# Performance work log

Hardware: AMD Instinct MI355X
Metric: run time of the kernel (lower is better)

Reference implementation:

```python
import jax, jax.numpy as jnp
import numpy as np

L, H, C = 2, 2, 128            # conv layers, heads, out_channels
N, E, B = 10000, 100000, 64    # nodes, edges, graphs
F_NODE, F_EDGE, FC = 92, 50, 512
HC, C3 = H * C, 3 * C


def _ln(x, g, b, eps=1e-5):
    m = x.mean(-1, keepdims=True)
    v = jnp.var(x, axis=-1, keepdims=True)
    return (x - m) * jax.lax.rsqrt(v + eps) * g + b


def setup_inputs() -> dict:
    key = jax.random.key(0)
    ks = jax.random.split(key, 20)
    r = lambda i, shape, s=0.05: jax.random.normal(ks[i], shape, jnp.float32) * s
    d = {}
    d["x"] = jax.random.normal(ks[0], (N, F_NODE), jnp.float32)
    d["edge_attr"] = jax.random.normal(ks[1], (E, F_EDGE), jnp.float32)
    d["pge"] = jax.random.normal(ks[2], (B, 32), jnp.float32)
    d["cse"] = jax.random.normal(ks[3], (B, 7), jnp.float32)
    d["edge_index"] = jax.random.randint(ks[4], (2, E), 0, N, jnp.int32)
    d["batch"] = jnp.sort(jax.random.randint(ks[5], (N,), 0, B, jnp.int32))
    d["atom_W"] = r(6, (F_NODE, C)); d["atom_b"] = jnp.zeros(C)
    d["edge_W"] = r(7, (F_EDGE, C)); d["edge_b"] = jnp.zeros(C)
    d["Wq"] = r(8, (L, C, HC)); d["bq"] = jnp.zeros((L, HC))
    d["Wk"] = r(9, (L, C, HC)); d["bk"] = jnp.zeros((L, HC))
    d["Wv"] = r(10, (L, C, HC)); d["bv"] = jnp.zeros((L, HC))
    d["We"] = r(11, (L, C, HC))
    d["Wmu"] = r(12, (L, C3, C3)); d["bmu"] = jnp.zeros((L, C3))
    d["Wm"] = r(13, (L, C3, C)); d["bm"] = jnp.zeros((L, C))
    d["ln_m_g"] = jnp.ones((L, C)); d["ln_m_b"] = jnp.zeros((L, C))
    d["ln_a_g"] = jnp.ones((L, C3)); d["ln_a_b"] = jnp.zeros((L, C3))
    d["Wc"] = r(14, (L, HC, C)); d["bc"] = jnp.zeros((L, C))
    d["bn_g"] = jnp.ones((L, C)); d["bn_b"] = jnp.zeros((L, C))
    d["Wskip"] = r(15, (L, C, C)); d["bskip"] = jnp.zeros((L, C))
    d["fc_W"] = r(16, (C + 32 + 7, FC)); d["fc_b"] = jnp.zeros(FC)
    d["out_W"] = r(17, (FC, 1)); d["out_b"] = jnp.zeros(1)
    return d


def reference(x, edge_attr, pge, cse, edge_index, batch, atom_W, atom_b,
              edge_W, edge_b, Wq, bq, Wk, bk, Wv, bv, We, Wmu, bmu, Wm, bm,
              ln_m_g, ln_m_b, ln_a_g, ln_a_b, Wc, bc, bn_g, bn_b, Wskip,
              bskip, fc_W, fc_b, out_W, out_b):
    src, dst = edge_index[0], edge_index[1]  # j = source, i = target
    nf = x @ atom_W + atom_b                 # [N, C]
    ef = edge_attr @ edge_W + edge_b         # [E, C]
    scale = 1.0 / np.sqrt(C3).astype(np.float32)
    for i in range(L):
        q = (nf @ Wq[i] + bq[i]).reshape(N, H, C)
        k = (nf @ Wk[i] + bk[i]).reshape(N, H, C)
        v = (nf @ Wv[i] + bv[i]).reshape(N, H, C)
        ea = (ef @ We[i]).reshape(E, H, C)
        qi = q[dst]
        qcat = jnp.concatenate([qi, qi, qi], -1)                 # [E,H,3C]
        kcat = jnp.concatenate([k[dst], k[src], ea], -1)         # [E,H,3C]
        alpha = qcat * kcat * scale
        gate = jax.nn.sigmoid(_ln(alpha, ln_a_g[i], ln_a_b[i]))
        m = jnp.concatenate([v[dst], v[src], ea], -1)            # [E,H,3C]
        m = (jnp.einsum('ehf,fg->ehg', m, Wmu[i]) + bmu[i]) * gate
        m = jnp.einsum('ehf,fc->ehc', m, Wm[i]) + bm[i]          # [E,H,C]
        m = _ln(m, ln_m_g[i], ln_m_b[i])
        agg = jax.ops.segment_sum(m, dst, num_segments=N)        # scatter-add
        o = agg.reshape(N, HC) @ Wc[i] + bc[i]                   # lin_concate
        mu = o.mean(0); var = jnp.var(o, axis=0)                 # BN (batch stats)
        o = (o - mu) * jax.lax.rsqrt(var + 1e-5) * bn_g[i] + bn_b[i]
        o = jax.nn.silu(o)
        nf = o + nf @ Wskip[i] + bskip[i]                        # root skip
    sums = jax.ops.segment_sum(nf, batch, num_segments=B)
    cnt = jax.ops.segment_sum(jnp.ones((N, 1), nf.dtype), batch, num_segments=B)
    pooled = sums / jnp.maximum(cnt, 1.0)                        # global_mean_pool
    feats = jnp.concatenate([pooled, pge, cse], 1)               # [B, C+39]
    h = jax.nn.silu(feats @ fc_W + fc_b)
    return h @ out_W + out_b                                     # [B, 1]
```

## Files before the change

kernel.cpp:

```cpp
#include <hip/hip_runtime.h>
#include <math.h>

#define N_NODES 10000
#define N_EDGES 100000
#define N_GRAPH 64
#define CDIM 128
#define HCDIM 256
#define C3DIM 384
#define QKPW 2176

typedef unsigned short u16;
typedef __attribute__((ext_vector_type(8))) short bf16x8;
typedef __attribute__((ext_vector_type(4))) float f32x4;

__device__ __forceinline__ u16 f2bf(float f) {
  union { float f; unsigned int u; } x; x.f = f;
  unsigned int u = x.u + 0x7fffu + ((x.u >> 16) & 1u);
  return (u16)(u >> 16);
}
__device__ __forceinline__ float bf2f(u16 h) {
  union { unsigned int u; float f; } x; x.u = ((unsigned int)h) << 16;
  return x.f;
}

template<int OUT_BF16, int DO_STATS, int A_F32>
__global__ __launch_bounds__(256) void mfma_gemm_kernel(
    const void* __restrict__ Ain, const u16* __restrict__ WT,
    const float* __restrict__ bias, void* __restrict__ Y,
    u16* __restrict__ Ymirror, float* __restrict__ cs, float* __restrict__ cs2,
    int M, int K, int N) {
  const int tid = threadIdx.x;
  const int w = tid >> 6, l = tid & 63;
  const int lq = l >> 4, ln = l & 15;
  const int bm = blockIdx.y * 128, bn = blockIdx.x * 64;
  int ra = bm + w * 32 + ln;      if (ra > M - 1) ra = M - 1;
  int rb = bm + w * 32 + 16 + ln; if (rb > M - 1) rb = M - 1;
  f32x4 acc[2][4];
#pragma unroll
  for (int g = 0; g < 2; ++g)
#pragma unroll
    for (int nt = 0; nt < 4; ++nt) acc[g][nt] = {0.f, 0.f, 0.f, 0.f};
  for (int k0 = 0; k0 < K; k0 += 32) {
    bf16x8 a0, a1;
    if (A_F32) {
      const float* Af = (const float*)Ain;
      f32x4 p0 = *(const f32x4*)&Af[(size_t)ra * K + k0 + lq * 8];
      f32x4 p1 = *(const f32x4*)&Af[(size_t)ra * K + k0 + lq * 8 + 4];
      f32x4 p2 = *(const f32x4*)&Af[(size_t)rb * K + k0 + lq * 8];
      f32x4 p3 = *(const f32x4*)&Af[(size_t)rb * K + k0 + lq * 8 + 4];
#pragma unroll
      for (int j = 0; j < 4; ++j) {
        a0[j] = (short)f2bf(p0[j]); a0[4 + j] = (short)f2bf(p1[j]);
        a1[j] = (short)f2bf(p2[j]); a1[4 + j] = (short)f2bf(p3[j]);
      }
    } else {
      const u16* Ab = (const u16*)Ain;
      a0 = *(const bf16x8*)&Ab[(size_t)ra * K + k0 + lq * 8];
      a1 = *(const bf16x8*)&Ab[(size_t)rb * K + k0 + lq * 8];
    }
#pragma unroll
    for (int nt = 0; nt < 4; ++nt) {
      bf16x8 b = *(const bf16x8*)&WT[(size_t)(bn + nt * 16 + ln) * K + k0 + lq * 8];
      acc[0][nt] = __builtin_amdgcn_mfma_f32_16x16x32_bf16(a0, b, acc[0][nt], 0, 0, 0);
      acc[1][nt] = __builtin_amdgcn_mfma_f32_16x16x32_bf16(a1, b, acc[1][nt], 0, 0, 0);
    }
  }
#pragma unroll
  for (int g = 0; g < 2; ++g) {
    int rowbase = bm + w * 32 + g * 16 + lq * 4;
#pragma unroll
    for (int nt = 0; nt < 4; ++nt) {
      int gn = bn + nt * 16 + ln;
      float bv = bias ? bias[gn] : 0.f;
#pragma unroll
      for (int r = 0; r < 4; ++r) {
        int gm = rowbase + r;
        if (gm < M) {
          float val = acc[g][nt][r] + bv;
          if (OUT_BF16) ((u16*)Y)[(size_t)gm * N + gn] = f2bf(val);
          else          ((float*)Y)[(size_t)gm * N + gn] = val;
          if (Ymirror)  Ymirror[(size_t)gm * N + gn] = f2bf(val);
        }
      }
    }
  }
  if (DO_STATS) {
#pragma unroll
    for (int nt = 0; nt < 4; ++nt) {
      int gn = bn + nt * 16 + ln;
      float bv = bias ? bias[gn] : 0.f;
      float s = 0.f, s2 = 0.f;
#pragma unroll
      for (int g = 0; g < 2; ++g) {
        int rowbase = bm + w * 32 + g * 16 + lq * 4;
#pragma unroll
        for (int r = 0; r < 4; ++r) {
          if (rowbase + r < M) {
            float v = acc[g][nt][r] + bv;
            s += v; s2 += v * v;
          }
        }
      }
      s += __shfl_xor(s, 16); s2 += __shfl_xor(s2, 16);
      s += __shfl_xor(s, 32); s2 += __shfl_xor(s2, 32);
      if (lq == 0) { atomicAdd(&cs[gn], s); atomicAdd(&cs2[gn], s2); }
    }
  }
}

__global__ void pack_init_kernel(
    const float* __restrict__ x, const float* __restrict__ ea,
    const float* __restrict__ atom_W, const float* __restrict__ edge_W,
    u16* __restrict__ xpad, u16* __restrict__ epad,
    u16* __restrict__ atomWT, u16* __restrict__ WeT2) {
  int z = blockIdx.y;
  int idx0 = blockIdx.x * 256 + threadIdx.x;
  const int stride = 256 * 256;
  if (z == 0) {
    for (int idx = idx0; idx < N_NODES * 96; idx += stride) {
      int n = idx / 96, k = idx - n * 96;
      xpad[idx] = (k < 92) ? f2bf(x[(size_t)n * 92 + k]) : (u16)0;
    }
  } else if (z == 1) {
    for (int idx = idx0; idx < N_EDGES * 64; idx += stride) {
      int e = idx >> 6, k = idx & 63;
      epad[idx] = (k < 50) ? f2bf(ea[(size_t)e * 50 + k]) : (u16)0;
    }
  } else if (z == 2) {
    if (idx0 < 128 * 96) { int n = idx0 / 96, k = idx0 - n * 96;
      atomWT[idx0] = (k < 92) ? f2bf(atom_W[(size_t)k * 128 + n]) : (u16)0; }
  } else {
    if (idx0 < 128 * 64) { int n = idx0 >> 6, k = idx0 & 63;
      WeT2[idx0] = (k < 50) ? f2bf(edge_W[(size_t)k * 128 + n]) : (u16)0; }
  }
}

__global__ __launch_bounds__(256) void prep_kernel(
    const float* __restrict__ Wv, const float* __restrict__ We_l,
    const float* __restrict__ Wmu,
    const float* __restrict__ Wq, const float* __restrict__ Wk,
    const float* __restrict__ Wc, const float* __restrict__ Wsk,
    const float* __restrict__ Wm_l, const float* __restrict__ bmu,
    const float* __restrict__ bv_l,
    const float* __restrict__ bq_l, const float* __restrict__ bk_l,
    const float* __restrict__ bsk_l,
    u16* __restrict__ WallT, u16* __restrict__ WcT, u16* __restrict__ WcTw,
    u16* __restrict__ WmTb, float* __restrict__ cbv, float* __restrict__ ball,
    float* __restrict__ agg, float* __restrict__ cs, float* __restrict__ cs2) {
  __shared__ float As[16][68];
  __shared__ float Bs[16][65];
  const int b = blockIdx.x;
  const int tid = threadIdx.x;
  if (b < 72) {
    const int zc = b / 12, rem = b % 12;
    const int by = rem / 6, bx = rem % 6;
    const float* Ap; const float* Bp; u16* Cp; int colbase;
    if (zc < 4) {
      int part = zc >> 1, h = zc & 1;
      Ap = Wv + h * 128; Bp = Wmu + part * 128 * 384;
      Cp = WallT; colbase = 512 + part * 768 + h * 384;
    } else {
      int h = zc - 4;
      Ap = We_l + h * 128; Bp = Wmu + 256 * 384;
      Cp = WcT; colbase = 256 + h * 384;
    }
    const int bm = by * 64, bn = bx * 64;
    const int tx = tid & 15, ty = tid >> 4;
    float acc[4][4] = {};
    for (int k0 = 0; k0 < 128; k0 += 16) {
#pragma unroll
      for (int i = 0; i < 4; ++i) {
        int l = tid + i * 256;
        int kk = l & 15, m = l >> 4;
        As[kk][m] = Ap[(size_t)(bm + m) * 256 + k0 + kk];
      }
#pragma unroll
      for (int i = 0; i < 4; ++i) {
        int l = tid + i * 256;
        int n = l & 63, kk = l >> 6;
        Bs[kk][n] = Bp[(size_t)(k0 + kk) * 384 + bn + n];
      }
      __syncthreads();
#pragma unroll
      for (int kk = 0; kk < 16; ++kk) {
        float a[4], bb[4];
#pragma unroll
        for (int i = 0; i < 4; ++i) a[i] = As[kk][ty * 4 + i];
#pragma unroll
        for (int j = 0; j < 4; ++j) bb[j] = Bs[kk][tx * 4 + j];
#pragma unroll
        for (int i = 0; i < 4; ++i)
#pragma unroll
          for (int j = 0; j < 4; ++j) acc[i][j] += a[i] * bb[j];
      }
      __syncthreads();
    }
#pragma unroll
    for (int i = 0; i < 4; ++i) {
      int gk = bm + ty * 4 + i;
#pragma unroll
      for (int j = 0; j < 4; ++j) {
        int gcol = colbase + bn + tx * 4 + j;
        Cp[(size_t)gcol * 128 + gk] = f2bf(acc[i][j]);
      }
    }
    return;
  }
  const int pb = b - 72;
  const int z = pb / 192;
  const int idx = (pb % 192) * 256 + tid;
  if (z == 0) {
    if (idx < 32768) { int col = idx >> 7, kk = idx & 127;
      WallT[(size_t)col * 128 + kk] = f2bf(Wq[(size_t)kk * 256 + col]); }
  } else if (z == 1) {
    if (idx < 32768) { int col = idx >> 7, kk = idx & 127;
      WallT[(size_t)(256 + col) * 128 + kk] = f2bf(Wk[(size_t)kk * 256 + col]); }
  } else if (z == 2) {
    if (idx < 32768) { int col = idx >> 8, kk = idx & 255;
      WcTw[(size_t)col * 256 + kk] = f2bf(Wc[(size_t)kk * 128 + col]); }
  } else if (z == 3) {
    if (idx < 16384) { int col = idx >> 7, kk = idx & 127;
      WallT[(size_t)(2048 + col) * 128 + kk] = f2bf(Wsk[(size_t)kk * 128 + col]); }
  } else if (z == 4) {
    if (idx < 49152) { int col = idx / 384, kk = idx - col * 384;
      WmTb[idx] = f2bf(Wm_l[(size_t)kk * 128 + col]); }
  } else if (z == 5) {
    if (idx < 768) {
      int h2 = idx / 384, g = idx - h2 * 384;
      float s = bmu[g];
      for (int d = 0; d < 128; ++d)
        s += bv_l[h2 * 128 + d] * (Wmu[(size_t)d * 384 + g] + Wmu[(size_t)(128 + d) * 384 + g]);
      cbv[idx] = s;
    }
  } else if (z == 6) {
    if (idx < QKPW) {
      float v = 0.f;
      if (idx < 256) v = bq_l[idx];
      else if (idx < 512) v = bk_l[idx - 256];
      else if (idx >= 2048) v = bsk_l[idx - 2048];
      ball[idx] = v;
    }
  } else if (z == 7) {
    for (int p = idx; p < N_NODES * HCDIM; p += 192 * 256) agg[p] = 0.f;
    if (idx < 128) { cs[idx] = 0.f; cs2[idx] = 0.f; }
  } else {
    if (idx < 32768) { int col = idx >> 7, kk = idx & 127;
      WcT[(size_t)col * 128 + kk] = f2bf(We_l[(size_t)kk * 256 + col]); }
  }
}

__global__ __launch_bounds__(256, 3) void edge_kernel(
    const u16* __restrict__ qkp, const u16* __restrict__ efb,
    const int* __restrict__ ei, const u16* __restrict__ WcT,
    const float* __restrict__ cbv,
    const float* __restrict__ lag, const float* __restrict__ lab,
    const u16* __restrict__ WmT, const float* __restrict__ bm_l,
    const float* __restrict__ lmg, const float* __restrict__ lmb,
    float* __restrict__ agg, int E) {
  __shared__ __align__(16) u16 C1[16 * 1032];
  __shared__ __align__(16) u16 A2p[12 * 512];
  __shared__ int did16[16];
  float* C2 = (float*)A2p;
  const int tid = threadIdx.x;
  const int e0 = blockIdx.x * 16;
  const int w = tid >> 6, l = tid & 63;
  const int lq = l >> 4, ln = l & 15;
  const float scale = 0.051031036307982884f;

  if (tid < 16) did16[tid] = ei[E + e0 + tid];

  const int r = tid >> 4, lx = tid & 15;
  const int hA = r >> 3, eA = r & 7;

  bf16x8 qv[2], kdv[2], ksv[2], pdv[2][3], psv[2][3];
#pragma unroll
  for (int s = 0; s < 2; ++s) {
    int edge = e0 + s * 8 + eA;
    int dstn = ei[E + edge], srcn = ei[edge];
    const u16* db = qkp + (size_t)dstn * QKPW;
    const u16* sb = qkp + (size_t)srcn * QKPW;
    qv[s]  = *(const bf16x8*)&db[hA * 128 + lx * 8];
    kdv[s] = *(const bf16x8*)&db[256 + hA * 128 + lx * 8];
    ksv[s] = *(const bf16x8*)&sb[256 + hA * 128 + lx * 8];
#pragma unroll
    for (int p = 0; p < 3; ++p) {
      pdv[s][p] = *(const bf16x8*)&db[512 + hA * 384 + p * 128 + lx * 8];
      psv[s][p] = *(const bf16x8*)&sb[512 + 768 + hA * 384 + p * 128 + lx * 8];
    }
  }

  {
    bf16x8 afr[4];
    const u16* ab = efb + (size_t)(e0 + ln) * 128 + lq * 8;
#pragma unroll
    for (int ks = 0; ks < 4; ++ks) afr[ks] = *(const bf16x8*)(ab + ks * 32);
    for (int nt = 0; nt < 16; ++nt) {
      int g = w * 16 + nt;
      const u16* bb = WcT + (size_t)(g * 16 + ln) * 128 + lq * 8;
      f32x4 acc = {0.f, 0.f, 0.f, 0.f};
#pragma unroll
      for (int ks = 0; ks < 4; ++ks)
        acc = __builtin_amdgcn_mfma_f32_16x16x32_bf16(
            afr[ks], *(const bf16x8*)(bb + ks * 32), acc, 0, 0, 0);
      int col = g * 16 + ln;
#pragma unroll
      for (int rr = 0; rr < 4; ++rr) C1[(lq * 4 + rr) * 1032 + col] = f2bf(acc[rr]);
    }
  }
  __syncthreads();

  for (int s = 0; s < 2; ++s) {
    {
      bf16x8 sea = *(const bf16x8*)&C1[(s * 8 + eA) * 1032 + hA * 128 + lx * 8];
      float a0[8], a1[8], a2[8];
      float sacc = 0.f, s2acc = 0.f;
#pragma unroll
      for (int j = 0; j < 8; ++j) {
        float qf = bf2f((u16)qv[s][j]);
        float x0 = qf * bf2f((u16)kdv[s][j]) * scale;
        float x1 = qf * bf2f((u16)ksv[s][j]) * scale;
        float x2 = qf * bf2f((u16)sea[j]) * scale;
        a0[j] = x0; a1[j] = x1; a2[j] = x2;
        sacc += x0 + x1 + x2;
        s2acc += x0 * x0 + x1 * x1 + x2 * x2;
      }
#pragma unroll
      for (int mm = 1; mm < 16; mm <<= 1) {
        sacc += __shfl_xor(sacc, mm); s2acc += __shfl_xor(s2acc, mm);
      }
      float mean = sacc * (1.f / C3DIM);
      float rstd = rsqrtf(s2acc * (1.f / C3DIM) - mean * mean + 1e-5f);
#pragma unroll
      for (int p = 0; p < 3; ++p) {
        const float* lg = lag + p * 128 + lx * 8;
        const float* lb = lab + p * 128 + lx * 8;
        f32x4 g0 = *(const f32x4*)lg, g1 = *(const f32x4*)(lg + 4);
        f32x4 b0 = *(const f32x4*)lb, b1 = *(const f32x4*)(lb + 4);
        f32x4 c0 = *(const f32x4*)&cbv[hA * 384 + p * 128 + lx * 8];
        f32x4 c1 = *(const f32x4*)&cbv[hA * 384 + p * 128 + lx * 8 + 4];
        bf16x8 pe = *(const bf16x8*)&C1[(s * 8 + eA) * 1032 + 256 + hA * 384 + p * 128 + lx * 8];
        bf16x8 outv;
#pragma unroll
        for (int j = 0; j < 8; ++j) {
          float av = p == 0 ? a0[j] : (p == 1 ? a1[j] : a2[j]);
          float gg = j < 4 ? g0[j] : g1[j - 4];
          float bb2 = j < 4 ? b0[j] : b1[j - 4];
          float cbj = j < 4 ? c0[j] : c1[j - 4];
          float z = (av - mean) * rstd * gg + bb2;
          float gate = 1.f / (1.f + expf(-z));
          float t = (bf2f((u16)pe[j]) + bf2f((u16)pdv[s][p][j]) +
                     bf2f((u16)psv[s][p][j]) + cbj) * gate;
          outv[j] = (short)f2bf(t);
        }
        int ks = p * 4 + (lx >> 2), qq = lx & 3;
        int slot = (((r ^ (qq << 2)) + ks) & 15) | (qq << 4);
        *(bf16x8*)&A2p[ks * 512 + slot * 8] = outv;
      }
    }
    __syncthreads();

    {
      bf16x8 af2[12];
#pragma unroll
      for (int ks = 0; ks < 12; ++ks) {
        int slot = (((ln ^ (lq << 2)) + ks) & 15) | (lq << 4);
        af2[ks] = *(const bf16x8*)&A2p[ks * 512 + slot * 8];
      }
      __syncthreads();
#pragma unroll
      for (int nt = 0; nt < 2; ++nt) {
        int g = w * 2 + nt;
        const u16* bb = WmT + (size_t)(g * 16 + ln) * 384 + lq * 8;
        f32x4 acc = {0.f, 0.f, 0.f, 0.f};
#pragma unroll
        for (int ks = 0; ks < 12; ++ks)
          acc = __builtin_amdgcn_mfma_f32_16x16x32_bf16(
              af2[ks], *(const bf16x8*)(bb + ks * 32), acc, 0, 0, 0);
        int col = g * 16 + ln;
        float bcol = bm_l[col];
#pragma unroll
        for (int rr = 0; rr < 4; ++rr) C2[(lq * 4 + rr) * 132 + col] = acc[rr] + bcol;
      }
    }
    __syncthreads();

    {
      for (int rw = w; rw < 16; rw += 4) {
        float v0 = C2[rw * 132 + l], v1 = C2[rw * 132 + l + 64];
        float sa = v0 + v1, s2a = v0 * v0 + v1 * v1;
#pragma unroll
        for (int off2 = 32; off2 > 0; off2 >>= 1) {
          sa += __shfl_down(sa, off2); s2a += __shfl_down(s2a, off2);
        }
        sa = __shfl(sa, 0); s2a = __shfl(s2a, 0);
        float mean = sa * (1.f / CDIM);
        float rstd = rsqrtf(s2a * (1.f / CDIM) - mean * mean + 1e-5f);
        int h = rw >> 3, e = rw & 7;
        int dstn = did16[s * 8 + e];
        float o0 = (v0 - mean) * rstd * lmg[l] + lmb[l];
        float o1 = (v1 - mean) * rstd * lmg[l + 64] + lmb[l + 64];
        atomicAdd(&agg[(size_t)dstn * HCDIM + h * CDIM + l], o0);
        atomicAdd(&agg[(size_t)dstn * HCDIM + h * CDIM + l + 64], o1);
      }
    }
    __syncthreads();
  }
}

__global__ void bn_silu_skip_kernel(
    const float* __restrict__ o, const u16* __restrict__ qkp,
    const float* __restrict__ cs, const float* __restrict__ cs2,
    const float* __restrict__ g, const float* __restrict__ b,
    float* __restrict__ nf, u16* __restrict__ nfb) {
  int idx = blockIdx.x * blockDim.x + threadIdx.x;
  if (idx >= N_NODES * CDIM) return;
  int c = idx & (CDIM - 1);
  int n = idx >> 7;
  float m = cs[c] * (1.f / N_NODES);
  float var = cs2[c] * (1.f / N_NODES) - m * m;
  float rstd = rsqrtf(var + 1e-5f);
  float x = (o[idx] - m) * rstd * g[c] + b[c];
  float sig = 1.f / (1.f + expf(-x));
  float skipv = bf2f(qkp[(size_t)n * QKPW + 2048 + c]);
  float val = x * sig + skipv;
  nf[idx] = val;
  nfb[idx] = f2bf(val);
}

__global__ __launch_bounds__(256) void poolfeats_kernel(
    const float* __restrict__ nf, const int* __restrict__ batch,
    const float* __restrict__ pge, const float* __restrict__ cse,
    float* __restrict__ feats) {
  const int b = blockIdx.x, tid = threadIdx.x;
  int lo = 0, hi = N_NODES;
  {
    int L = 0, R = N_NODES;
    while (L < R) { int m2 = (L + R) >> 1; if (batch[m2] < b) L = m2 + 1; else R = m2; }
    lo = L;
    L = lo; R = N_NODES;
    while (L < R) { int m2 = (L + R) >> 1; if (batch[m2] <= b) L = m2 + 1; else R = m2; }
    hi = L;
  }
  __shared__ float sacc[2][128];
  const int half = tid >> 7, c = tid & 127;
  float s = 0.f;
  for (int n = lo + half; n < hi; n += 2) s += nf[(size_t)n * CDIM + c];
  sacc[half][c] = s;
  __syncthreads();
  float cntf = fmaxf((float)(hi - lo), 1.f);
  if (tid < 128) feats[b * 167 + tid] = (sacc[0][tid] + sacc[1][tid]) / cntf;
  else if (tid < 160) feats[b * 167 + 128 + (tid - 128)] = pge[b * 32 + (tid - 128)];
  else if (tid < 167) feats[b * 167 + 160 + (tid - 160)] = cse[b * 7 + (tid - 160)];
}

__global__ __launch_bounds__(256) void fcout_kernel(
    const float* __restrict__ feats, const float* __restrict__ fc_W,
    const float* __restrict__ fc_b, const float* __restrict__ ow,
    const float* __restrict__ ob, float* __restrict__ out) {
  const int b = blockIdx.x, tid = threadIdx.x;
  __shared__ float sf[167];
  if (tid < 167) sf[tid] = feats[b * 167 + tid];
  __syncthreads();
  float acc0 = fc_b[tid], acc1 = fc_b[tid + 256];
  for (int k = 0; k < 167; ++k) {
    float fv = sf[k];
    acc0 += fv * fc_W[(size_t)k * 512 + tid];
    acc1 += fv * fc_W[(size_t)k * 512 + tid + 256];
  }
  float h0 = acc0 / (1.f + expf(-acc0));
  float h1 = acc1 / (1.f + expf(-acc1));
  float s = h0 * ow[tid] + h1 * ow[tid + 256];
  __shared__ float red[4];
#pragma unroll
  for (int off = 32; off > 0; off >>= 1) s += __shfl_down(s, off);
  if ((tid & 63) == 0) red[tid >> 6] = s;
  __syncthreads();
  if (tid == 0) out[b] = red[0] + red[1] + red[2] + red[3] + ob[0];
}

extern "C" void kernel_launch(void* const* d_in, const int* in_sizes, int n_in,
                              void* d_out, int out_size, void* d_ws, size_t ws_size,
                              hipStream_t stream) {
  const float* x         = (const float*)d_in[0];
  const float* edge_attr = (const float*)d_in[1];
  const float* pge       = (const float*)d_in[2];
  const float* cse       = (const float*)d_in[3];
  const int*   ei        = (const int*)d_in[4];
  const int*   batch     = (const int*)d_in[5];
  const float* atom_W    = (const float*)d_in[6];
  const float* atom_b    = (const float*)d_in[7];
  const float* edge_W    = (const float*)d_in[8];
  const float* edge_b    = (const float*)d_in[9];
  const float* Wq        = (const float*)d_in[10];
  const float* bq        = (const float*)d_in[11];
  const float* Wk        = (const float*)d_in[12];
  const float* bk        = (const float*)d_in[13];
  const float* Wv        = (const float*)d_in[14];
  const float* bv        = (const float*)d_in[15];
  const float* We        = (const float*)d_in[16];
  const float* Wmu       = (const float*)d_in[17];
  const float* bmu       = (const float*)d_in[18];
  const float* Wm        = (const float*)d_in[19];
  const float* bm        = (const float*)d_in[20];
  const float* ln_m_g    = (const float*)d_in[21];
  const float* ln_m_b    = (const float*)d_in[22];
  const float* ln_a_g    = (const float*)d_in[23];
  const float* ln_a_b    = (const float*)d_in[24];
  const float* Wc        = (const float*)d_in[25];
  const float* bc        = (const float*)d_in[26];
  const float* bn_g      = (const float*)d_in[27];
  const float* bn_b      = (const float*)d_in[28];
  const float* Wskip     = (const float*)d_in[29];
  const float* bskip     = (const float*)d_in[30];
  const float* fc_W      = (const float*)d_in[31];
  const float* fc_b      = (const float*)d_in[32];
  const float* out_W     = (const float*)d_in[33];
  const float* out_b     = (const float*)d_in[34];

  float* ws = (float*)d_ws;
  size_t off = 0;
  float* nf    = ws + off; off += (size_t)N_NODES * CDIM;
  float* agg   = ws + off; off += (size_t)N_NODES * HCDIM;
  float* o     = ws + off; off += (size_t)N_NODES * CDIM;
  float* cbv   = ws + off; off += 768;
  float* ball  = ws + off; off += QKPW;
  float* csum  = ws + off; off += CDIM;
  float* csum2 = ws + off; off += CDIM;
  float* feats = ws + off; off += (size_t)N_GRAPH * 167;
  u16* efb   = (u16*)(ws + off); off += (size_t)N_EDGES * 64;
  u16* WcT   = (u16*)(ws + off); off += 65536;
  u16* WmTb  = (u16*)(ws + off); off += 24576;
  u16* nfb   = (u16*)(ws + off); off += (size_t)N_NODES * 64;
  u16* qkp   = (u16*)(ws + off); off += (size_t)N_NODES * (QKPW/2);
  u16* WallT = (u16*)(ws + off); off += (size_t)QKPW * 64;
  u16* WcTw  = (u16*)(ws + off); off += 16384;
  u16* xpad  = (u16*)(ws + off); off += (size_t)N_NODES * 48;
  u16* epad  = (u16*)(ws + off); off += (size_t)N_EDGES * 32;
  u16* atomWT= (u16*)(ws + off); off += 6144;
  u16* WeT2  = (u16*)(ws + off); off += 4096;

  pack_init_kernel<<<dim3(256, 4), 256, 0, stream>>>(x, edge_attr, atom_W, edge_W,
                                                     xpad, epad, atomWT, WeT2);
  mfma_gemm_kernel<0, 0, 0><<<dim3(2, 79), 256, 0, stream>>>(
      xpad, atomWT, atom_b, nf, nfb, nullptr, nullptr, N_NODES, 96, CDIM);
  mfma_gemm_kernel<1, 0, 0><<<dim3(2, 782), 256, 0, stream>>>(
      epad, WeT2, edge_b, efb, nullptr, nullptr, nullptr, N_EDGES, 64, CDIM);

  for (int i = 0; i < 2; ++i) {
    prep_kernel<<<dim3(1800), 256, 0, stream>>>(
        Wv + (size_t)i * CDIM * HCDIM, We + (size_t)i * CDIM * HCDIM,
        Wmu + (size_t)i * C3DIM * C3DIM,
        Wq + (size_t)i * CDIM * HCDIM, Wk + (size_t)i * CDIM * HCDIM,
        Wc + (size_t)i * HCDIM * CDIM, Wskip + (size_t)i * CDIM * CDIM,
        Wm + (size_t)i * C3DIM * CDIM, bmu + i * C3DIM, bv + i * HCDIM,
        bq + i * HCDIM, bk + i * HCDIM, bskip + i * CDIM,
        WallT, WcT, WcTw, WmTb, cbv, ball, agg, csum, csum2);

    mfma_gemm_kernel<1, 0, 0><<<dim3(QKPW / 64, 79), 256, 0, stream>>>(
        nfb, WallT, ball, qkp, nullptr, nullptr, nullptr, N_NODES, CDIM, QKPW);

    edge_kernel<<<dim3(N_EDGES / 16), dim3(256), 0, stream>>>(
        qkp, efb, ei, WcT, cbv,
        ln_a_g + i * C3DIM, ln_a_b + i * C3DIM,
        WmTb, bm + i * CDIM,
        ln_m_g + i * CDIM, ln_m_b + i * CDIM, agg, N_EDGES);

    mfma_gemm_kernel<0, 1, 1><<<dim3(2, 79), 256, 0, stream>>>(
        agg, WcTw, bc + i * CDIM, o, nullptr, csum, csum2, N_NODES, HCDIM, CDIM);

    bn_silu_skip_kernel<<<dim3((N_NODES * CDIM + 255) / 256), dim3(256), 0, stream>>>(
        o, qkp, csum, csum2, bn_g + i * CDIM, bn_b + i * CDIM, nf, nfb);
  }

  poolfeats_kernel<<<dim3(N_GRAPH), 256, 0, stream>>>(nf, batch, pge, cse, feats);
  fcout_kernel<<<dim3(N_GRAPH), 256, 0, stream>>>(feats, fc_W, fc_b, out_W, out_b,
                                                  (float*)d_out);
}
```

Measured before the change: 1.218 ms.

## Split edge kernel per head across blocks to halve per-block LDS and registers

The edge kernel now gives each head to a separate block, so grid size doubles and each block handles 16 edges for one head instead of both heads in two serial passes. The edge-feature projection computes only that head's 512 columns, which halves the C1 shared buffer, and launch bounds are raised to allow more resident blocks per CU. The goal is higher occupancy and better latency hiding. In exchange, each edge's efb row and indices are loaded twice and the per-block fixed costs are repeated across twice as many blocks.

```diff
diff --git a/kernel.cpp b/kernel.cpp
--- a/kernel.cpp
+++ b/kernel.cpp
@@ -249,7 +249,8 @@
   }
 }
 
-__global__ __launch_bounds__(256, 3) void edge_kernel(
+#define C1S 520
+__global__ __launch_bounds__(256, 5) void edge_kernel(
     const u16* __restrict__ qkp, const u16* __restrict__ efb,
     const int* __restrict__ ei, const u16* __restrict__ WcT,
     const float* __restrict__ cbv,
@@ -257,12 +258,13 @@
     const u16* __restrict__ WmT, const float* __restrict__ bm_l,
     const float* __restrict__ lmg, const float* __restrict__ lmb,
     float* __restrict__ agg, int E) {
-  __shared__ __align__(16) u16 C1[16 * 1032];
+  __shared__ __align__(16) u16 C1[16 * C1S];
   __shared__ __align__(16) u16 A2p[12 * 512];
   __shared__ int did16[16];
   float* C2 = (float*)A2p;
   const int tid = threadIdx.x;
-  const int e0 = blockIdx.x * 16;
+  const int h = blockIdx.x & 1;
+  const int e0 = (blockIdx.x >> 1) * 16;
   const int w = tid >> 6, l = tid & 63;
   const int lq = l >> 4, ln = l & 15;
   const float scale = 0.051031036307982884f;
@@ -270,22 +272,20 @@
   if (tid < 16) did16[tid] = ei[E + e0 + tid];
 
   const int r = tid >> 4, lx = tid & 15;
-  const int hA = r >> 3, eA = r & 7;
-
-  bf16x8 qv[2], kdv[2], ksv[2], pdv[2][3], psv[2][3];
-#pragma unroll
-  for (int s = 0; s < 2; ++s) {
-    int edge = e0 + s * 8 + eA;
+
+  bf16x8 qv, kdv, ksv, pdv[3], psv[3];
+  {
+    int edge = e0 + r;
     int dstn = ei[E + edge], srcn = ei[edge];
     const u16* db = qkp + (size_t)dstn * QKPW;
     const u16* sb = qkp + (size_t)srcn * QKPW;
-    qv[s]  = *(const bf16x8*)&db[hA * 128 + lx * 8];
-    kdv[s] = *(const bf16x8*)&db[256 + hA * 128 + lx * 8];
-    ksv[s] = *(const bf16x8*)&sb[256 + hA * 128 + lx * 8];
+    qv  = *(const bf16x8*)&db[h * 128 + lx * 8];
+    kdv = *(const bf16x8*)&db[256 + h * 128 + lx * 8];
+    ksv = *(const bf16x8*)&sb[256 + h * 128 + lx * 8];
 #pragma unroll
     for (int p = 0; p < 3; ++p) {
-      pdv[s][p] = *(const bf16x8*)&db[512 + hA * 384 + p * 128 + lx * 8];
-      psv[s][p] = *(const bf16x8*)&sb[512 + 768 + hA * 384 + p * 128 + lx * 8];
+      pdv[p] = *(const bf16x8*)&db[512 + h * 384 + p * 128 + lx * 8];
+      psv[p] = *(const bf16x8*)&sb[512 + 768 + h * 384 + p * 128 + lx * 8];
     }
   }
 
@@ -294,116 +294,114 @@
     const u16* ab = efb + (size_t)(e0 + ln) * 128 + lq * 8;
 #pragma unroll
     for (int ks = 0; ks < 4; ++ks) afr[ks] = *(const bf16x8*)(ab + ks * 32);
-    for (int nt = 0; nt < 16; ++nt) {
-      int g = w * 16 + nt;
-      const u16* bb = WcT + (size_t)(g * 16 + ln) * 128 + lq * 8;
+#pragma unroll 2
+    for (int nt = 0; nt < 8; ++nt) {
+      int col0 = (w * 8 + nt) * 16;
+      int wc = (col0 < 128) ? h * 128 + col0 : 256 + h * 384 + (col0 - 128);
+      const u16* bb = WcT + (size_t)(wc + ln) * 128 + lq * 8;
       f32x4 acc = {0.f, 0.f, 0.f, 0.f};
 #pragma unroll
       for (int ks = 0; ks < 4; ++ks)
         acc = __builtin_amdgcn_mfma_f32_16x16x32_bf16(
             afr[ks], *(const bf16x8*)(bb + ks * 32), acc, 0, 0, 0);
+      int col = col0 + ln;
+#pragma unroll
+      for (int rr = 0; rr < 4; ++rr) C1[(lq * 4 + rr) * C1S + col] = f2bf(acc[rr]);
+    }
+  }
+  __syncthreads();
+
+  {
+    bf16x8 sea = *(const bf16x8*)&C1[r * C1S + lx * 8];
+    float a0[8], a1[8], a2[8];
+    float sacc = 0.f, s2acc = 0.f;
+#pragma unroll
+    for (int j = 0; j < 8; ++j) {
+      float qf = bf2f((u16)qv[j]);
+      float x0 = qf * bf2f((u16)kdv[j]) * scale;
+      float x1 = qf * bf2f((u16)ksv[j]) * scale;
+      float x2 = qf * bf2f((u16)sea[j]) * scale;
+      a0[j] = x0; a1[j] = x1; a2[j] = x2;
+      sacc += x0 + x1 + x2;
+      s2acc += x0 * x0 + x1 * x1 + x2 * x2;
+    }
+#pragma unroll
+    for (int mm = 1; mm < 16; mm <<= 1) {
+      sacc += __shfl_xor(sacc, mm); s2acc += __shfl_xor(s2acc, mm);
+    }
+    float mean = sacc * (1.f / C3DIM);
+    float rstd = rsqrtf(s2acc * (1.f / C3DIM) - mean * mean + 1e-5f);
+#pragma unroll
+    for (int p = 0; p < 3; ++p) {
+      const float* lg = lag + p * 128 + lx * 8;
+      const float* lb = lab + p * 128 + lx * 8;
+      f32x4 g0 = *(const f32x4*)lg, g1 = *(const f32x4*)(lg + 4);
+      f32x4 b0 = *(const f32x4*)lb, b1 = *(const f32x4*)(lb + 4);
+      f32x4 c0 = *(const f32x4*)&cbv[h * 384 + p * 128 + lx * 8];
+      f32x4 c1 = *(const f32x4*)&cbv[h * 384 + p * 128 + lx * 8 + 4];
+      bf16x8 pe = *(const bf16x8*)&C1[r * C1S + 128 + p * 128 + lx * 8];
+      bf16x8 outv;
+#pragma unroll
+      for (int j = 0; j < 8; ++j) {
+        float av = p == 0 ? a0[j] : (p == 1 ? a1[j] : a2[j]);
+        float gg = j < 4 ? g0[j] : g1[j - 4];
+        float bb2 = j < 4 ? b0[j] : b1[j - 4];
+        float cbj = j < 4 ? c0[j] : c1[j - 4];
+        float z = (av - mean) * rstd * gg + bb2;
+        float gate = 1.f / (1.f + expf(-z));
+        float t = (bf2f((u16)pe[j]) + bf2f((u16)pdv[p][j]) +
+                   bf2f((u16)psv[p][j]) + cbj) * gate;
+        outv[j] = (short)f2bf(t);
+      }
+      int ks = p * 4 + (lx >> 2), qq = lx & 3;
+      int slot = (((r ^ (qq << 2)) + ks) & 15) | (qq << 4);
+      *(bf16x8*)&A2p[ks * 512 + slot * 8] = outv;
+    }
+  }
+  __syncthreads();
+
+  {
+    bf16x8 af2[12];
+#pragma unroll
+    for (int ks = 0; ks < 12; ++ks) {
+      int slot = (((ln ^ (lq << 2)) + ks) & 15) | (lq << 4);
+      af2[ks] = *(const bf16x8*)&A2p[ks * 512 + slot * 8];
+    }
+    __syncthreads();
+#pragma unroll
+    for (int nt = 0; nt < 2; ++nt) {
+      int g = w * 2 + nt;
+      const u16* bb = WmT + (size_t)(g * 16 + ln) * 384 + lq * 8;
+      f32x4 acc = {0.f, 0.f, 0.f, 0.f};
+#pragma unroll
+      for (int ks = 0; ks < 12; ++ks)
+        acc = __builtin_amdgcn_mfma_f32_16x16x32_bf16(
+            af2[ks], *(const bf16x8*)(bb + ks * 32), acc, 0, 0, 0);
       int col = g * 16 + ln;
-#pragma unroll
-      for (int rr = 0; rr < 4; ++rr) C1[(lq * 4 + rr) * 1032 + col] = f2bf(acc[rr]);
+      float bcol = bm_l[col];
+#pragma unroll
+      for (int rr = 0; rr < 4; ++rr) C2[(lq * 4 + rr) * 132 + col] = acc[rr] + bcol;
     }
   }
   __syncthreads();
 
-  for (int s = 0; s < 2; ++s) {
-    {
-      bf16x8 sea = *(const bf16x8*)&C1[(s * 8 + eA) * 1032 + hA * 128 + lx * 8];
-      float a0[8], a1[8], a2[8];
-      float sacc = 0.f, s2acc = 0.f;
-#pragma unroll
-      for (int j = 0; j < 8; ++j) {
-        float qf = bf2f((u16)qv[s][j]);
-        float x0 = qf * bf2f((u16)kdv[s][j]) * scale;
-        float x1 = qf * bf2f((u16)ksv[s][j]) * scale;
-        float x2 = qf * bf2f((u16)sea[j]) * scale;
-        a0[j] = x0; a1[j] = x1; a2[j] = x2;
-        sacc += x0 + x1 + x2;
-        s2acc += x0 * x0 + x1 * x1 + x2 * x2;
-      }
-#pragma unroll
-      for (int mm = 1; mm < 16; mm <<= 1) {
-        sacc += __shfl_xor(sacc, mm); s2acc += __shfl_xor(s2acc, mm);
-      }
-      float mean = sacc * (1.f / C3DIM);
-      float rstd = rsqrtf(s2acc * (1.f / C3DIM) - mean * mean + 1e-5f);
-#pragma unroll
-      for (int p = 0; p < 3; ++p) {
-        const float* lg = lag + p * 128 + lx * 8;
-        const float* lb = lab + p * 128 + lx * 8;
-        f32x4 g0 = *(const f32x4*)lg, g1 = *(const f32x4*)(lg + 4);
-        f32x4 b0 = *(const f32x4*)lb, b1 = *(const f32x4*)(lb + 4);
-        f32x4 c0 = *(const f32x4*)&cbv[hA * 384 + p * 128 + lx * 8];
-        f32x4 c1 = *(const f32x4*)&cbv[hA * 384 + p * 128 + lx * 8 + 4];
-        bf16x8 pe = *(const bf16x8*)&C1[(s * 8 + eA) * 1032 + 256 + hA * 384 + p * 128 + lx * 8];
-        bf16x8 outv;
-#pragma unroll
-        for (int j = 0; j < 8; ++j) {
-          float av = p == 0 ? a0[j] : (p == 1 ? a1[j] : a2[j]);
-          float gg = j < 4 ? g0[j] : g1[j - 4];
-          float bb2 = j < 4 ? b0[j] : b1[j - 4];
-          float cbj = j < 4 ? c0[j] : c1[j - 4];
-          float z = (av - mean) * rstd * gg + bb2;
-          float gate = 1.f / (1.f + expf(-z));
-          float t = (bf2f((u16)pe[j]) + bf2f((u16)pdv[s][p][j]) +
-                     bf2f((u16)psv[s][p][j]) + cbj) * gate;
-          outv[j] = (short)f2bf(t);
-        }
-        int ks = p * 4 + (lx >> 2), qq = lx & 3;
-        int slot = (((r ^ (qq << 2)) + ks) & 15) | (qq << 4);
-        *(bf16x8*)&A2p[ks * 512 + slot * 8] = outv;
-      }
-    }
-    __syncthreads();
-
-    {
-      bf16x8 af2[12];
-#pragma unroll
-      for (int ks = 0; ks < 12; ++ks) {
-        int slot = (((ln ^ (lq << 2)) + ks) & 15) | (lq << 4);
-        af2[ks] = *(const bf16x8*)&A2p[ks * 512 + slot * 8];
-      }
-      __syncthreads();
-#pragma unroll
-      for (int nt = 0; nt < 2; ++nt) {
-        int g = w * 2 + nt;
-        const u16* bb = WmT + (size_t)(g * 16 + ln) * 384 + lq * 8;
-        f32x4 acc = {0.f, 0.f, 0.f, 0.f};
-#pragma unroll
-        for (int ks = 0; ks < 12; ++ks)
-          acc = __builtin_amdgcn_mfma_f32_16x16x32_bf16(
-              af2[ks], *(const bf16x8*)(bb + ks * 32), acc, 0, 0, 0);
-        int col = g * 16 + ln;
-        float bcol = bm_l[col];
-#pragma unroll
-        for (int rr = 0; rr < 4; ++rr) C2[(lq * 4 + rr) * 132 + col] = acc[rr] + bcol;
-      }
-    }
-    __syncthreads();
-
-    {
-      for (int rw = w; rw < 16; rw += 4) {
-        float v0 = C2[rw * 132 + l], v1 = C2[rw * 132 + l + 64];
-        float sa = v0 + v1, s2a = v0 * v0 + v1 * v1;
-#pragma unroll
-        for (int off2 = 32; off2 > 0; off2 >>= 1) {
-          sa += __shfl_down(sa, off2); s2a += __shfl_down(s2a, off2);
-        }
-        sa = __shfl(sa, 0); s2a = __shfl(s2a, 0);
-        float mean = sa * (1.f / CDIM);
-        float rstd = rsqrtf(s2a * (1.f / CDIM) - mean * mean + 1e-5f);
-        int h = rw >> 3, e = rw & 7;
-        int dstn = did16[s * 8 + e];
-        float o0 = (v0 - mean) * rstd * lmg[l] + lmb[l];
-        float o1 = (v1 - mean) * rstd * lmg[l + 64] + lmb[l + 64];
-        atomicAdd(&agg[(size_t)dstn * HCDIM + h * CDIM + l], o0);
-        atomicAdd(&agg[(size_t)dstn * HCDIM + h * CDIM + l + 64], o1);
-      }
-    }
-    __syncthreads();
+  {
+    for (int rw = w; rw < 16; rw += 4) {
+      float v0 = C2[rw * 132 + l], v1 = C2[rw * 132 + l + 64];
+      float sa = v0 + v1, s2a = v0 * v0 + v1 * v1;
+#pragma unroll
+      for (int off2 = 32; off2 > 0; off2 >>= 1) {
+        sa += __shfl_down(sa, off2); s2a += __shfl_down(s2a, off2);
+      }
+      sa = __shfl(sa, 0); s2a = __shfl(s2a, 0);
+      float mean = sa * (1.f / CDIM);
+      float rstd = rsqrtf(s2a * (1.f / CDIM) - mean * mean + 1e-5f);
+      int dstn = did16[rw];
+      float o0 = (v0 - mean) * rstd * lmg[l] + lmb[l];
+      float o1 = (v1 - mean) * rstd * lmg[l + 64] + lmb[l + 64];
+      atomicAdd(&agg[(size_t)dstn * HCDIM + h * CDIM + l], o0);
+      atomicAdd(&agg[(size_t)dstn * HCDIM + h * CDIM + l + 64], o1);
+    }
   }
 }
 
@@ -559,7 +557,7 @@
     mfma_gemm_kernel<1, 0, 0><<<dim3(QKPW / 64, 79), 256, 0, stream>>>(
         nfb, WallT, ball, qkp, nullptr, nullptr, nullptr, N_NODES, CDIM, QKPW);
 
-    edge_kernel<<<dim3(N_EDGES / 16), dim3(256), 0, stream>>>(
+    edge_kernel<<<dim3(N_EDGES / 16 * 2), dim3(256), 0, stream>>>(
         qkp, efb, ei, WcT, cbv,
         ln_a_g + i * C3DIM, ln_a_b + i * C3DIM,
         WmTb, bm + i * CDIM,
```

Measured after the change: 1.171 ms. 1.04x faster.
